# Performance work log

Hardware: AMD Instinct MI355X
Metric: run time of the kernel (lower is better)

The kernel has to match this reference:

```python
import jax, jax.numpy as jnp
import numpy as np

N_NODES = 50000
N_EDGES = 800000
IN_CH, HID_CH, OUT_CH = 128, 128, 64


def setup_inputs() -> dict:
    key = jax.random.key(0)
    k1, k2, k3, k4, k5, k6 = jax.random.split(key, 6)
    x = jax.random.normal(k1, (N_NODES, IN_CH), dtype=jnp.float32)
    edge_index = jax.random.randint(k2, (2, N_EDGES), 0, N_NODES, dtype=jnp.int64)
    # nn.Linear params: W [out, in], b [out]
    W1 = jax.random.normal(k3, (HID_CH, IN_CH), dtype=jnp.float32) / np.sqrt(IN_CH)
    b1 = jax.random.normal(k4, (HID_CH,), dtype=jnp.float32) * 0.01
    W2 = jax.random.normal(k5, (OUT_CH, HID_CH), dtype=jnp.float32) / np.sqrt(HID_CH)
    b2 = jax.random.normal(k6, (OUT_CH,), dtype=jnp.float32) * 0.01
    return {"x": x, "edge_index": edge_index, "W1": W1, "b1": b1, "W2": W2, "b2": b2}


def _aggregate(x, edge_index):
    # Faithful to SimpleGNN.aggregate: deg from ROW counts, normalization gathered at DST (col).
    row, col = edge_index[0], edge_index[1]
    n = x.shape[0]
    deg = jnp.bincount(row, length=n).astype(x.dtype)
    deg_inv = jnp.where(deg > 0, 1.0 / deg, 0.0)
    # out[dst] += x[src] * deg_inv[dst]  ==  segment_sum(x[src] by dst) * deg_inv[dst]
    agg = jax.ops.segment_sum(x[row], col, num_segments=n)
    return agg * deg_inv[:, None]


def reference(x, edge_index, W1, b1, W2, b2):
    h = x @ W1.T + b1                 # [N, hidden]
    h = _aggregate(h, edge_index)     # degree-normalized scatter-add
    out = h @ W2.T + b2               # [N, out]
    return out
```

## Files before the change

kernel.cpp:

```cpp
#include <hip/hip_runtime.h>
#include <hip/hip_bf16.h>


#define IN_CH   128
#define OUT_CH  64
#define NCHUNK  64
#define NRANGE  8
#define RBINS   6272
#define MC_BLOCKS 33
#define MC_PAD  40
#define YROWS   32
#define PLACE_BLOCKS (NCHUNK * NRANGE)
#define SMEM_FLOATS (IN_CH * OUT_CH + YROWS * (IN_CH + 4))

typedef unsigned short u16;
typedef unsigned int u32;

static __device__ inline float bfu32_lo(u32 u) { return __uint_as_float(u << 16); }
static __device__ inline float bfu32_hi(u32 u) { return __uint_as_float(u & 0xffff0000u); }
static __device__ inline u16 f2bf(float f) {
    __hip_bfloat16 h = __float2bfloat16(f);
    return *reinterpret_cast<u16*>(&h);
}

static __device__ inline int detect_stride_wave(const int* __restrict__ ei) {
    int lane = threadIdx.x & 63;
    int idx = (lane < 32) ? (2 * lane + 1) : 1;
    int v = ei[idx];
    unsigned long long m = __ballot((v != 0) && (lane < 32));
    return (m == 0ull) ? 2 : 1;
}

__global__ __launch_bounds__(256) void mk_prep(const float* __restrict__ W1,
                                               const float* __restrict__ b1,
                                               const float* __restrict__ W2,
                                               const int* __restrict__ ei,
                                               float* __restrict__ M,
                                               float* __restrict__ c,
                                               u16* __restrict__ row_slab,
                                               u16* __restrict__ col_slab,
                                               int n_edges, int n_nodes) {
    __shared__ u32 bins[RBINS];
    int b = blockIdx.x;
    int tid = threadIdx.x;
    if (b < MC_PAD) {
        int t = b * 256 + tid;
        if (t < IN_CH * OUT_CH) {
            int o = t & (OUT_CH - 1);
            int i = t >> 6;
            float acc = 0.f;
            for (int h = 0; h < 128; ++h)
                acc += W1[h * 128 + i] * W2[o * 128 + h];
            M[i * OUT_CH + o] = acc;
        } else if (t < IN_CH * OUT_CH + OUT_CH) {
            int o = t - IN_CH * OUT_CH;
            float acc = 0.f;
            for (int h = 0; h < 128; ++h)
                acc += b1[h] * W2[o * 128 + h];
            c[o] = acc;
        }
        return;
    }
    int hb = b - MC_PAD;
    int range = hb & (NRANGE - 1);
    int chunk = hb >> 3;

    int range_size = (n_nodes + NRANGE - 1) / NRANGE;
    int lo = range * range_size;
    int hi = lo + range_size; if (hi > n_nodes) hi = n_nodes;
    int nbins = hi - lo;
    if (nbins <= 0) return;

    int stride = detect_stride_wave(ei);
    for (int i = tid; i < nbins; i += 256) bins[i] = 0u;
    __syncthreads();

    size_t e0 = (size_t)chunk * n_edges / NCHUNK;
    size_t e1 = (size_t)(chunk + 1) * n_edges / NCHUNK;
    size_t cnt = e1 - e0;
    const int* rp = ei;
    const int* cp = ei + (size_t)n_edges * stride;

    size_t i = tid;
    int s[8], d[8];
    for (; i + 1792 < cnt; i += 2048) {
#pragma unroll
        for (int k = 0; k < 8; ++k) s[k] = rp[(e0 + i + 256 * k) * stride];
#pragma unroll
        for (int k = 0; k < 8; ++k) d[k] = cp[(e0 + i + 256 * k) * stride];
#pragma unroll
        for (int k = 0; k < 8; ++k) {
            if (s[k] >= lo && s[k] < hi) atomicAdd(&bins[s[k] - lo], 1u);
            if (d[k] >= lo && d[k] < hi && (unsigned)s[k] < (unsigned)n_nodes)
                atomicAdd(&bins[d[k] - lo], 0x10000u);
        }
    }
    for (; i < cnt; i += 256) {
        int ss = rp[(e0 + i) * stride];
        int dd = cp[(e0 + i) * stride];
        if (ss >= lo && ss < hi) atomicAdd(&bins[ss - lo], 1u);
        if (dd >= lo && dd < hi && (unsigned)ss < (unsigned)n_nodes)
            atomicAdd(&bins[dd - lo], 0x10000u);
    }
    __syncthreads();

    size_t base = (size_t)chunk * n_nodes + lo;
    for (int k = tid; k < nbins; k += 256) {
        u32 v = bins[k];
        row_slab[base + k] = (u16)(v & 0xFFFFu);
        col_slab[base + k] = (u16)(v >> 16);
    }
}

__global__ __launch_bounds__(256) void mk_choff(u16* __restrict__ row_slab,
                                                u16* __restrict__ col_slab,
                                                int* __restrict__ deg_row,
                                                int* __restrict__ cnt_col,
                                                int* __restrict__ cursor_part,
                                                int* __restrict__ bsums,
                                                int n_nodes) {
    __shared__ int sm[256];
    int t = threadIdx.x;
    int n = blockIdx.x * 256 + t;
    int run = 0;
    if (n < n_nodes) {
        int sum = 0;
#pragma unroll 8
        for (int ch = 0; ch < NCHUNK; ++ch)
            sum += row_slab[(size_t)ch * n_nodes + n];
        deg_row[n] = sum;
#pragma unroll 8
        for (int ch = 0; ch < NCHUNK; ++ch) {
            int v = col_slab[(size_t)ch * n_nodes + n];
            col_slab[(size_t)ch * n_nodes + n] = (u16)run;
            run += v;
        }
        cnt_col[n] = run;
    }
    sm[t] = run;
    __syncthreads();
    for (int d = 1; d < 256; d <<= 1) {
        int add = (t >= d) ? sm[t - d] : 0;
        __syncthreads();
        sm[t] += add;
        __syncthreads();
    }
    if (n < n_nodes) cursor_part[n] = sm[t] - run;
    if (t == 255) bsums[blockIdx.x] = sm[t];
}

static __device__ void block_bscan(const int* __restrict__ bsums, int nb,
                                   int* __restrict__ bscan) {
    int t = threadIdx.x;
    int v = (t < nb) ? bsums[t] : 0;
    bscan[t] = v;
    __syncthreads();
    for (int d = 1; d < 256; d <<= 1) {
        int add = (t >= d) ? bscan[t - d] : 0;
        __syncthreads();
        bscan[t] += add;
        __syncthreads();
    }
    bscan[t] -= v;
    __syncthreads();
}

__global__ __launch_bounds__(256) void mk_place_y(const int* __restrict__ ei,
                                                  const int* __restrict__ cursor_part,
                                                  const int* __restrict__ bsums,
                                                  const u16* __restrict__ col_slab,
                                                  int* __restrict__ csr_src,
                                                  const float* __restrict__ x,
                                                  const float* __restrict__ M,
                                                  u16* __restrict__ y,
                                                  int n_edges, int n_nodes, int nb) {
    __shared__ float smem[SMEM_FLOATS];
    int b = blockIdx.x;
    int tid = threadIdx.x;

    if (b < PLACE_BLOCKS) {
        int* rank = (int*)smem;
        int* bscan = (int*)smem + RBINS;
        block_bscan(bsums, nb, bscan);

        int range = b & (NRANGE - 1);
        int chunk = b >> 3;
        int range_size = (n_nodes + NRANGE - 1) / NRANGE;
        int lo = range * range_size;
        int hi = lo + range_size; if (hi > n_nodes) hi = n_nodes;
        if (hi <= lo) return;

        int stride = detect_stride_wave(ei);
        for (int i = tid; i < hi - lo; i += 256) rank[i] = 0;
        __syncthreads();

        size_t e0 = (size_t)chunk * n_edges / NCHUNK;
        size_t e1 = (size_t)(chunk + 1) * n_edges / NCHUNK;
        size_t cnt = e1 - e0;
        const int* rp = ei;
        const int* cp = ei + (size_t)n_edges * stride;
        size_t slab_base = (size_t)chunk * n_nodes;

        size_t i = tid;
        int s[8], d[8], cpart[8], coff[8];
        for (; i + 1792 < cnt; i += 2048) {
#pragma unroll
            for (int k = 0; k < 8; ++k) s[k] = rp[(e0 + i + 256 * k) * stride];
#pragma unroll
            for (int k = 0; k < 8; ++k) d[k] = cp[(e0 + i + 256 * k) * stride];
#pragma unroll
            for (int k = 0; k < 8; ++k) {
                int dc = (d[k] >= lo && d[k] < hi) ? d[k] : lo;
                cpart[k] = cursor_part[dc];
                coff[k]  = (int)col_slab[slab_base + dc];
            }
#pragma unroll
            for (int k = 0; k < 8; ++k) {
                if (d[k] >= lo && d[k] < hi && (unsigned)s[k] < (unsigned)n_nodes) {
                    int r = atomicAdd(&rank[d[k] - lo], 1);
                    csr_src[cpart[k] + bscan[d[k] >> 8] + coff[k] + r] = s[k];
                }
            }
        }
        for (; i < cnt; i += 256) {
            int ss = rp[(e0 + i) * stride];
            int dd = cp[(e0 + i) * stride];
            if (dd >= lo && dd < hi && (unsigned)ss < (unsigned)n_nodes) {
                int r = atomicAdd(&rank[dd - lo], 1);
                csr_src[cursor_part[dd] + bscan[dd >> 8] + (int)col_slab[slab_base + dd] + r] = ss;
            }
        }
        return;
    }

    int t = b - PLACE_BLOCKS;
    float* Ms = smem;
    float (*xs)[IN_CH + 4] = (float(*)[IN_CH + 4])(smem + IN_CH * OUT_CH);
    int tx = tid & 15;
    int ty = tid >> 4;
    int row0 = t * YROWS;
    if (row0 >= n_nodes) return;

    const float4* Mv = (const float4*)M;
    float4* Msv = (float4*)Ms;
#pragma unroll
    for (int k = 0; k < 8; ++k) Msv[tid + 256 * k] = Mv[tid + 256 * k];

    for (int f = tid; f < YROWS * 32; f += 256) {
        int r = f >> 5, kq = f & 31;
        float4 v = make_float4(0.f, 0.f, 0.f, 0.f);
        if (row0 + r < n_nodes)
            v = *(const float4*)&x[(size_t)(row0 + r) * IN_CH + 4 * kq];
        *(float4*)&xs[r][4 * kq] = v;
    }
    __syncthreads();

    float4 acc0 = make_float4(0.f, 0.f, 0.f, 0.f);
    float4 acc1 = make_float4(0.f, 0.f, 0.f, 0.f);

    for (int k = 0; k < IN_CH; k += 4) {
        float4 xr0 = *(const float4*)&xs[ty][k];
        float4 xr1 = *(const float4*)&xs[ty + 16][k];
        float4 m0 = *(const float4*)&Ms[(k + 0) * OUT_CH + 4 * tx];
        float4 m1 = *(const float4*)&Ms[(k + 1) * OUT_CH + 4 * tx];
        float4 m2 = *(const float4*)&Ms[(k + 2) * OUT_CH + 4 * tx];
        float4 m3 = *(const float4*)&Ms[(k + 3) * OUT_CH + 4 * tx];
        acc0.x = fmaf(xr0.x, m0.x, acc0.x); acc0.y = fmaf(xr0.x, m0.y, acc0.y);
        acc0.z = fmaf(xr0.x, m0.z, acc0.z); acc0.w = fmaf(xr0.x, m0.w, acc0.w);
        acc0.x = fmaf(xr0.y, m1.x, acc0.x); acc0.y = fmaf(xr0.y, m1.y, acc0.y);
        acc0.z = fmaf(xr0.y, m1.z, acc0.z); acc0.w = fmaf(xr0.y, m1.w, acc0.w);
        acc0.x = fmaf(xr0.z, m2.x, acc0.x); acc0.y = fmaf(xr0.z, m2.y, acc0.y);
        acc0.z = fmaf(xr0.z, m2.z, acc0.z); acc0.w = fmaf(xr0.z, m2.w, acc0.w);
        acc0.x = fmaf(xr0.w, m3.x, acc0.x); acc0.y = fmaf(xr0.w, m3.y, acc0.y);
        acc0.z = fmaf(xr0.w, m3.z, acc0.z); acc0.w = fmaf(xr0.w, m3.w, acc0.w);
        acc1.x = fmaf(xr1.x, m0.x, acc1.x); acc1.y = fmaf(xr1.x, m0.y, acc1.y);
        acc1.z = fmaf(xr1.x, m0.z, acc1.z); acc1.w = fmaf(xr1.x, m0.w, acc1.w);
        acc1.x = fmaf(xr1.y, m1.x, acc1.x); acc1.y = fmaf(xr1.y, m1.y, acc1.y);
        acc1.z = fmaf(xr1.y, m1.z, acc1.z); acc1.w = fmaf(xr1.y, m1.w, acc1.w);
        acc1.x = fmaf(xr1.z, m2.x, acc1.x); acc1.y = fmaf(xr1.z, m2.y, acc1.y);
        acc1.z = fmaf(xr1.z, m2.z, acc1.z); acc1.w = fmaf(xr1.z, m2.w, acc1.w);
        acc1.x = fmaf(xr1.w, m3.x, acc1.x); acc1.y = fmaf(xr1.w, m3.y, acc1.y);
        acc1.z = fmaf(xr1.w, m3.z, acc1.z); acc1.w = fmaf(xr1.w, m3.w, acc1.w);
    }

    int r0 = row0 + ty;
    int r1 = row0 + ty + 16;
    if (r0 < n_nodes) {
        ushort4 s4;
        s4.x = f2bf(acc0.x); s4.y = f2bf(acc0.y);
        s4.z = f2bf(acc0.z); s4.w = f2bf(acc0.w);
        *(ushort4*)&y[(size_t)r0 * OUT_CH + 4 * tx] = s4;
    }
    if (r1 < n_nodes) {
        ushort4 s4;
        s4.x = f2bf(acc1.x); s4.y = f2bf(acc1.y);
        s4.z = f2bf(acc1.z); s4.w = f2bf(acc1.w);
        *(ushort4*)&y[(size_t)r1 * OUT_CH + 4 * tx] = s4;
    }
}

__global__ __launch_bounds__(256) void mk_agg_final(const int* __restrict__ cursor_part,
                                                    const int* __restrict__ bsums,
                                                    const int* __restrict__ cnt_col,
                                                    const int* __restrict__ csr_src,
                                                    const int* __restrict__ deg_row,
                                                    const uint2* __restrict__ yv,
                                                    const float* __restrict__ c,
                                                    const float* __restrict__ b2,
                                                    float* __restrict__ out,
                                                    int n_nodes, int nb) {
    __shared__ int bscan[256];
    block_bscan(bsums, nb, bscan);

    int wave = threadIdx.x >> 6;
    int lane = threadIdx.x & 63;
    int dsub = lane >> 4;
    int ch   = lane & 15;
    int d = blockIdx.x * 16 + wave * 4 + dsub;
    if (d >= n_nodes) return;

    int start = cursor_part[d] + bscan[d >> 8];
    int cnt = cnt_col[d];
    int end = start + cnt;
    int e1m = end - 1;
    float a0 = 0.f, a1 = 0.f, a2 = 0.f, a3 = 0.f;
    for (int j = start; j < end; j += 8) {
        int idx[8], srcs[8];
#pragma unroll
        for (int k = 0; k < 8; ++k) {
            int t = j + k;
            idx[k] = t > e1m ? e1m : t;
        }
#pragma unroll
        for (int k = 0; k < 8; ++k) srcs[k] = csr_src[idx[k]];
        uint2 u[8];
#pragma unroll
        for (int k = 0; k < 8; ++k) u[k] = yv[(size_t)srcs[k] * 16 + ch];
#pragma unroll
        for (int k = 1; k < 8; ++k)
            if (j + k >= end) { u[k].x = 0u; u[k].y = 0u; }
#pragma unroll
        for (int k = 0; k < 8; ++k) {
            a0 += bfu32_lo(u[k].x);
            a1 += bfu32_hi(u[k].x);
            a2 += bfu32_lo(u[k].y);
            a3 += bfu32_hi(u[k].y);
        }
    }
    int dr = deg_row[d];
    float di = (dr > 0) ? (1.0f / (float)dr) : 0.f;
    float fc = di * (float)cnt;
    float4 cv = ((const float4*)c)[ch];
    float4 bv = ((const float4*)b2)[ch];
    float4 o;
    o.x = di * a0 + fc * cv.x + bv.x;
    o.y = di * a1 + fc * cv.y + bv.y;
    o.z = di * a2 + fc * cv.z + bv.z;
    o.w = di * a3 + fc * cv.w + bv.w;
    ((float4*)(out + (size_t)d * OUT_CH))[ch] = o;
}

extern "C" void kernel_launch(void* const* d_in, const int* in_sizes, int n_in,
                              void* d_out, int out_size, void* d_ws, size_t ws_size,
                              hipStream_t stream) {
    const float* x  = (const float*)d_in[0];
    const int*   ei = (const int*)d_in[1];
    const float* W1 = (const float*)d_in[2];
    const float* b1 = (const float*)d_in[3];
    const float* W2 = (const float*)d_in[4];
    const float* b2 = (const float*)d_in[5];
    float* out = (float*)d_out;

    const int n_nodes = in_sizes[0] / IN_CH;
    const int n_edges = in_sizes[1] / 2;

    const size_t slab_bytes = (((size_t)NCHUNK * n_nodes * 2) + 127) & ~(size_t)127;
    const size_t csr_bytes  = ((size_t)n_edges * 4 + 127) & ~(size_t)127;

    char* ws = (char*)d_ws;
    float* M        = (float*)(ws);
    float* c        = (float*)(ws + 32768);
    int*   deg_row  = (int*)  (ws + 33152);
    int*   cnt_col  = (int*)  (ws + 233216);
    int*   cursor   = (int*)  (ws + 433280);
    int*   bsums    = (int*)  (ws + 633344);
    u16*   row_slab = (u16*)  (ws + 637440);
    u16*   col_slab = (u16*)  (ws + 637440 + slab_bytes);
    int*   csr_src  = (int*)  (ws + 637440 + 2 * slab_bytes);
    u16*   y        = (u16*)  (ws + 637440 + 2 * slab_bytes + csr_bytes);

    const int y_blocks = (n_nodes + YROWS - 1) / YROWS;
    const int nb = (n_nodes + 255) / 256;

    mk_prep<<<MC_PAD + NCHUNK * NRANGE, 256, 0, stream>>>(
        W1, b1, W2, ei, M, c, row_slab, col_slab, n_edges, n_nodes);

    mk_choff<<<nb, 256, 0, stream>>>(row_slab, col_slab, deg_row, cnt_col,
                                     cursor, bsums, n_nodes);

    mk_place_y<<<PLACE_BLOCKS + y_blocks, 256, 0, stream>>>(
        ei, cursor, bsums, col_slab, csr_src, x, M, y, n_edges, n_nodes, nb);

    mk_agg_final<<<(n_nodes + 15) / 16, 256, 0, stream>>>(
        cursor, bsums, cnt_col, csr_src, deg_row, (const uint2*)y, c, b2, out,
        n_nodes, nb);
}
```

Baseline: 155.4 us.

## Record per-edge rank during histogram to drop atomics in placement pass

The histogram kernel now saves the pre-increment value of each destination-bin atomic as a per-edge 16-bit rank. The placement kernel reads that rank back, so it no longer re-scans every edge per node range or recomputes ranks with shared-memory atomics. Placement blocks instead split each chunk's edges into 8 disjoint sub-ranges, so each edge is read once rather than once per range. The cost is an extra per-edge u16 write and read through workspace, plus global lookups of cursor_part and col_slab across the full node range, which gives less locality.

Measured after the change: 164.5 us. 5.9% more time.

```diff
diff --git a/kernel.cpp b/kernel.cpp
--- a/kernel.cpp
+++ b/kernel.cpp
@@ -10,7 +10,7 @@
 #define MC_BLOCKS 33
 #define MC_PAD  40
 #define YROWS   32
-#define PLACE_BLOCKS (NCHUNK * NRANGE)
+#define PLACE_BLOCKS 512
 #define SMEM_FLOATS (IN_CH * OUT_CH + YROWS * (IN_CH + 4))
 
 typedef unsigned short u16;
@@ -39,6 +39,7 @@
                                                float* __restrict__ c,
                                                u16* __restrict__ row_slab,
                                                u16* __restrict__ col_slab,
+                                               u16* __restrict__ erank,
                                                int n_edges, int n_nodes) {
     __shared__ u32 bins[RBINS];
     int b = blockIdx.x;
@@ -91,16 +92,20 @@
 #pragma unroll
         for (int k = 0; k < 8; ++k) {
             if (s[k] >= lo && s[k] < hi) atomicAdd(&bins[s[k] - lo], 1u);
-            if (d[k] >= lo && d[k] < hi && (unsigned)s[k] < (unsigned)n_nodes)
-                atomicAdd(&bins[d[k] - lo], 0x10000u);
+            if (d[k] >= lo && d[k] < hi && (unsigned)s[k] < (unsigned)n_nodes) {
+                u32 old = atomicAdd(&bins[d[k] - lo], 0x10000u);
+                erank[e0 + i + 256 * k] = (u16)(old >> 16);
+            }
         }
     }
     for (; i < cnt; i += 256) {
         int ss = rp[(e0 + i) * stride];
         int dd = cp[(e0 + i) * stride];
         if (ss >= lo && ss < hi) atomicAdd(&bins[ss - lo], 1u);
-        if (dd >= lo && dd < hi && (unsigned)ss < (unsigned)n_nodes)
-            atomicAdd(&bins[dd - lo], 0x10000u);
+        if (dd >= lo && dd < hi && (unsigned)ss < (unsigned)n_nodes) {
+            u32 old = atomicAdd(&bins[dd - lo], 0x10000u);
+            erank[e0 + i] = (u16)(old >> 16);
+        }
     }
     __syncthreads();
 
@@ -169,6 +174,7 @@
                                                   const int* __restrict__ cursor_part,
                                                   const int* __restrict__ bsums,
                                                   const u16* __restrict__ col_slab,
+                                                  const u16* __restrict__ erank,
                                                   int* __restrict__ csr_src,
                                                   const float* __restrict__ x,
                                                   const float* __restrict__ M,
@@ -179,55 +185,46 @@
     int tid = threadIdx.x;
 
     if (b < PLACE_BLOCKS) {
-        int* rank = (int*)smem;
-        int* bscan = (int*)smem + RBINS;
+        int* bscan = (int*)smem;
         block_bscan(bsums, nb, bscan);
 
-        int range = b & (NRANGE - 1);
         int chunk = b >> 3;
-        int range_size = (n_nodes + NRANGE - 1) / NRANGE;
-        int lo = range * range_size;
-        int hi = lo + range_size; if (hi > n_nodes) hi = n_nodes;
-        if (hi <= lo) return;
-
+        int sub = b & 7;
         int stride = detect_stride_wave(ei);
-        for (int i = tid; i < hi - lo; i += 256) rank[i] = 0;
-        __syncthreads();
 
         size_t e0 = (size_t)chunk * n_edges / NCHUNK;
         size_t e1 = (size_t)(chunk + 1) * n_edges / NCHUNK;
         size_t cnt = e1 - e0;
+        size_t s0 = (size_t)sub * cnt / 8;
+        size_t s1 = (size_t)(sub + 1) * cnt / 8;
         const int* rp = ei;
         const int* cp = ei + (size_t)n_edges * stride;
         size_t slab_base = (size_t)chunk * n_nodes;
 
-        size_t i = tid;
-        int s[8], d[8], cpart[8], coff[8];
-        for (; i + 1792 < cnt; i += 2048) {
-#pragma unroll
-            for (int k = 0; k < 8; ++k) s[k] = rp[(e0 + i + 256 * k) * stride];
-#pragma unroll
-            for (int k = 0; k < 8; ++k) d[k] = cp[(e0 + i + 256 * k) * stride];
-#pragma unroll
-            for (int k = 0; k < 8; ++k) {
-                int dc = (d[k] >= lo && d[k] < hi) ? d[k] : lo;
-                cpart[k] = cursor_part[dc];
-                coff[k]  = (int)col_slab[slab_base + dc];
-            }
-#pragma unroll
-            for (int k = 0; k < 8; ++k) {
-                if (d[k] >= lo && d[k] < hi && (unsigned)s[k] < (unsigned)n_nodes) {
-                    int r = atomicAdd(&rank[d[k] - lo], 1);
-                    csr_src[cpart[k] + bscan[d[k] >> 8] + coff[k] + r] = s[k];
+        size_t i = s0 + tid;
+        for (; i + 768 < s1; i += 1024) {
+            int s4[4], d4[4]; u16 r4[4];
+#pragma unroll
+            for (int k = 0; k < 4; ++k) s4[k] = rp[(e0 + i + 256 * k) * stride];
+#pragma unroll
+            for (int k = 0; k < 4; ++k) d4[k] = cp[(e0 + i + 256 * k) * stride];
+#pragma unroll
+            for (int k = 0; k < 4; ++k) r4[k] = erank[e0 + i + 256 * k];
+#pragma unroll
+            for (int k = 0; k < 4; ++k) {
+                if ((unsigned)d4[k] < (unsigned)n_nodes &&
+                    (unsigned)s4[k] < (unsigned)n_nodes) {
+                    csr_src[cursor_part[d4[k]] + bscan[d4[k] >> 8] +
+                            (int)col_slab[slab_base + d4[k]] + (int)r4[k]] = s4[k];
                 }
             }
         }
-        for (; i < cnt; i += 256) {
+        for (; i < s1; i += 256) {
             int ss = rp[(e0 + i) * stride];
             int dd = cp[(e0 + i) * stride];
-            if (dd >= lo && dd < hi && (unsigned)ss < (unsigned)n_nodes) {
-                int r = atomicAdd(&rank[dd - lo], 1);
-                csr_src[cursor_part[dd] + bscan[dd >> 8] + (int)col_slab[slab_base + dd] + r] = ss;
+            if ((unsigned)dd < (unsigned)n_nodes && (unsigned)ss < (unsigned)n_nodes) {
+                csr_src[cursor_part[dd] + bscan[dd >> 8] +
+                        (int)col_slab[slab_base + dd] + (int)erank[e0 + i]] = ss;
             }
         }
         return;
@@ -376,6 +373,7 @@
 
     const size_t slab_bytes = (((size_t)NCHUNK * n_nodes * 2) + 127) & ~(size_t)127;
     const size_t csr_bytes  = ((size_t)n_edges * 4 + 127) & ~(size_t)127;
+    const size_t y_bytes    = ((size_t)n_nodes * OUT_CH * 2 + 127) & ~(size_t)127;
 
     char* ws = (char*)d_ws;
     float* M        = (float*)(ws);
@@ -388,18 +386,19 @@
     u16*   col_slab = (u16*)  (ws + 637440 + slab_bytes);
     int*   csr_src  = (int*)  (ws + 637440 + 2 * slab_bytes);
     u16*   y        = (u16*)  (ws + 637440 + 2 * slab_bytes + csr_bytes);
+    u16*   erank    = (u16*)  (ws + 637440 + 2 * slab_bytes + csr_bytes + y_bytes);
 
     const int y_blocks = (n_nodes + YROWS - 1) / YROWS;
     const int nb = (n_nodes + 255) / 256;
 
     mk_prep<<<MC_PAD + NCHUNK * NRANGE, 256, 0, stream>>>(
-        W1, b1, W2, ei, M, c, row_slab, col_slab, n_edges, n_nodes);
+        W1, b1, W2, ei, M, c, row_slab, col_slab, erank, n_edges, n_nodes);
 
     mk_choff<<<nb, 256, 0, stream>>>(row_slab, col_slab, deg_row, cnt_col,
                                      cursor, bsums, n_nodes);
 
     mk_place_y<<<PLACE_BLOCKS + y_blocks, 256, 0, stream>>>(
-        ei, cursor, bsums, col_slab, csr_src, x, M, y, n_edges, n_nodes, nb);
+        ei, cursor, bsums, col_slab, erank, csr_src, x, M, y, n_edges, n_nodes, nb);
 
     mk_agg_final<<<(n_nodes + 15) / 16, 256, 0, stream>>>(
         cursor, bsums, cnt_col, csr_src, deg_row, (const uint2*)y, c, b2, out,
```
